# Kernel optimization log

Measured on AMD Instinct MI355X. Metric: run time of the kernel, lower is better.

Reference implementation:

```python
import jax, jax.numpy as jnp
import numpy as np

NEG_SLOPE = 0.01  # torch.nn.LeakyReLU default


def setup_inputs() -> dict:
    key = jax.random.key(0)
    ks = jax.random.split(key, 9)
    B, S, F1, F2, N, M, E, L = 2, 256, 512, 512, 20000, 2, 320000, 3
    x = jax.random.normal(ks[0], (B, S, F1), dtype=jnp.float32)
    nodes = jax.random.normal(ks[1], (N, M, F2), dtype=jnp.float32)
    edge_index = jax.random.randint(ks[2], (2, E), 0, N, dtype=jnp.int32)
    Wp = jax.random.normal(ks[3], (F1, F2), dtype=jnp.float32) * 0.02  # torch Linear weight [out,in]
    bp = jax.random.normal(ks[4], (F1,), dtype=jnp.float32) * 0.02
    gcn_W = jax.random.normal(ks[5], (L, S, S), dtype=jnp.float32) * 0.05  # stored as [in,out]
    gcn_b = jax.random.normal(ks[6], (L, S), dtype=jnp.float32) * 0.02
    w_bp = jax.random.normal(ks[7], (S,), dtype=jnp.float32) * 0.05
    b_bp = jax.random.normal(ks[8], (1,), dtype=jnp.float32) * 0.02
    return {"x": x, "nodes": nodes, "edge_index": edge_index, "Wp": Wp, "bp": bp,
            "gcn_W": gcn_W, "gcn_b": gcn_b, "w_bp": w_bp, "b_bp": b_bp}


def reference(x, nodes, edge_index, Wp, bp, gcn_W, gcn_b, w_bp, b_bp):
    # Eval mode: dropout layers are identity.
    N = nodes.shape[0]
    L = gcn_W.shape[0]
    proj = nodes @ Wp.T + bp                         # [N, M, F1]
    score = jnp.einsum('bsk,nmk->bsn', x, proj)      # sum over M and F1 -> [B, S, N]
    h = score.transpose(0, 2, 1)                     # beliefs [B, N, S]

    # GCN normalization with self-loops: D^{-1/2} (A + I) D^{-1/2}
    src, dst = edge_index[0], edge_index[1]
    loop = jnp.arange(N, dtype=edge_index.dtype)
    row = jnp.concatenate([src, loop])               # message sources
    col = jnp.concatenate([dst, loop])               # message targets
    deg = jnp.zeros((N,), dtype=h.dtype).at[col].add(1.0)
    dinv = deg ** -0.5                               # deg >= 1 due to self-loops
    norm = dinv[row] * dinv[col]                     # [E+N]

    for l in range(L):
        hw = h @ gcn_W[l]                            # [B, N, S]
        msg = hw[:, row, :] * norm[None, :, None]    # gather + scale
        agg = jnp.zeros_like(hw).at[:, col, :].add(msg) + gcn_b[l]
        h = jax.nn.leaky_relu(agg, NEG_SLOPE)

    # belief_projection: Linear(S, 1) then squeeze -> [B, N]
    return h @ w_bp + b_bp[0]
```

## Files before the change

### kernel.cpp

```cpp
#include <hip/hip_runtime.h>
#include <cstddef>
#include <cstdint>

#define NN 20000

typedef short frag16 __attribute__((ext_vector_type(8)));
typedef float f32x4 __attribute__((ext_vector_type(4)));

__device__ inline unsigned short f32_to_bf16(float f) {
    uint32_t u = __float_as_uint(f);
    u += 0x7FFFu + ((u >> 16) & 1u);
    return (unsigned short)(u >> 16);
}

__device__ inline void dec8_add(uint4 v, float* a) {
    a[0] += __uint_as_float(v.x << 16);
    a[1] += __uint_as_float(v.x & 0xffff0000u);
    a[2] += __uint_as_float(v.y << 16);
    a[3] += __uint_as_float(v.y & 0xffff0000u);
    a[4] += __uint_as_float(v.z << 16);
    a[5] += __uint_as_float(v.z & 0xffff0000u);
    a[6] += __uint_as_float(v.w << 16);
    a[7] += __uint_as_float(v.w & 0xffff0000u);
}

__global__ __launch_bounds__(256) void prep(
    const float* __restrict__ nodes, const float* __restrict__ x,
    const float* __restrict__ gcn_W, const float* __restrict__ bp,
    const int* __restrict__ src, const int* __restrict__ dst,
    unsigned short* __restrict__ nsum16, unsigned short* __restrict__ WT,
    float* __restrict__ Tf, float* __restrict__ cvec,
    int* __restrict__ cnt, int* __restrict__ csr, int E)
{
    __shared__ __align__(16) char shmem[8704];
    const int blk = blockIdx.x, tid = threadIdx.x;

    if (blk < 64) {
        float* As = (float*)shmem;
        float* Bs = As + 1024;
        int t = blk;
        int b = t >> 5, rem = t & 31;
        int s0 = (rem >> 3) * 64, f0 = (rem & 7) * 64;
        const float* W1 = gcn_W;
        const float* xb = x + (size_t)b * 256 * 512;
        int kk = tid >> 4, c4 = (tid & 15) << 2;
        int tm = tid >> 4, tn = tid & 15;
        float acc[4][4] = {};
        float4 av = *(const float4*)(W1 + (size_t)kk * 256 + s0 + c4);
        float4 bv = *(const float4*)(xb + (size_t)kk * 512 + f0 + c4);
        for (int k0 = 0; k0 < 256; k0 += 16) {
            __syncthreads();
            *(float4*)&As[kk * 64 + c4] = av;
            *(float4*)&Bs[kk * 64 + c4] = bv;
            __syncthreads();
            if (k0 + 16 < 256) {
                av = *(const float4*)(W1 + (size_t)(k0 + 16 + kk) * 256 + s0 + c4);
                bv = *(const float4*)(xb + (size_t)(k0 + 16 + kk) * 512 + f0 + c4);
            }
            #pragma unroll
            for (int k = 0; k < 16; ++k) {
                float a[4], bb[4];
                *(float4*)a  = *(const float4*)&As[k * 64 + (tm << 2)];
                *(float4*)bb = *(const float4*)&Bs[k * 64 + (tn << 2)];
                #pragma unroll
                for (int i = 0; i < 4; ++i)
                    #pragma unroll
                    for (int j = 0; j < 4; ++j) acc[i][j] += a[i] * bb[j];
            }
        }
        #pragma unroll
        for (int i = 0; i < 4; ++i) {
            int row = b * 256 + s0 + (tm << 2) + i;
            *(float4*)(Tf + (size_t)row * 512 + f0 + (tn << 2)) =
                make_float4(acc[i][0], acc[i][1], acc[i][2], acc[i][3]);
        }
    } else if (blk < 96) {
        unsigned short (*tsh)[68] = (unsigned short(*)[68])shmem;
        int t = blk - 64;
        int l = t >> 4, rem = t & 15;
        int c0 = (rem & 3) * 64, r0 = (rem >> 2) * 64;
        const float* inp = gcn_W + (size_t)(l + 1) * 65536;
        unsigned short* outp = WT + (size_t)l * 65536;
        int tx = tid & 15, ty = tid >> 4;
        #pragma unroll
        for (int rr = 0; rr < 4; ++rr) {
            int r = ty * 4 + rr;
            float4 v = *(const float4*)(inp + (size_t)(r0 + r) * 256 + c0 + tx * 4);
            tsh[tx * 4 + 0][r] = f32_to_bf16(v.x);
            tsh[tx * 4 + 1][r] = f32_to_bf16(v.y);
            tsh[tx * 4 + 2][r] = f32_to_bf16(v.z);
            tsh[tx * 4 + 3][r] = f32_to_bf16(v.w);
        }
        __syncthreads();
        #pragma unroll
        for (int cc = 0; cc < 4; ++cc) {
            int c = ty * 4 + cc;
            ushort4 o = *(ushort4*)&tsh[c][tx * 4];
            *(ushort4*)(outp + (size_t)(c0 + c) * 256 + r0 + tx * 4) = o;
        }
    } else if (blk < 224) {
        int row = (blk - 96) * 4 + (tid >> 6);
        int lane = tid & 63;
        const float* xr = x + (size_t)row * 512;
        float s = 0.f;
        #pragma unroll
        for (int k = 0; k < 512; k += 64) s += xr[k + lane] * bp[k + lane];
        #pragma unroll
        for (int off = 32; off; off >>= 1) s += __shfl_down(s, off);
        if (lane == 0) cvec[row] = 2.0f * s;
    } else if (blk < 224 + 2512) {
        int g = (blk - 224) * 256 + tid;
        int n = g >> 5, c = (g & 31) << 4;
        uint4 o0, o1;
        if (n < NN) {
            const float* r0 = nodes + (size_t)n * 1024 + c;
            const float* r1 = r0 + 512;
            float4 a0 = *(const float4*)(r0 + 0),  a1 = *(const float4*)(r0 + 4);
            float4 a2 = *(const float4*)(r0 + 8),  a3 = *(const float4*)(r0 + 12);
            float4 b0 = *(const float4*)(r1 + 0),  b1 = *(const float4*)(r1 + 4);
            float4 b2 = *(const float4*)(r1 + 8),  b3 = *(const float4*)(r1 + 12);
            o0.x = ((uint32_t)f32_to_bf16(a0.y + b0.y) << 16) | f32_to_bf16(a0.x + b0.x);
            o0.y = ((uint32_t)f32_to_bf16(a0.w + b0.w) << 16) | f32_to_bf16(a0.z + b0.z);
            o0.z = ((uint32_t)f32_to_bf16(a1.y + b1.y) << 16) | f32_to_bf16(a1.x + b1.x);
            o0.w = ((uint32_t)f32_to_bf16(a1.w + b1.w) << 16) | f32_to_bf16(a1.z + b1.z);
            o1.x = ((uint32_t)f32_to_bf16(a2.y + b2.y) << 16) | f32_to_bf16(a2.x + b2.x);
            o1.y = ((uint32_t)f32_to_bf16(a2.w + b2.w) << 16) | f32_to_bf16(a2.z + b2.z);
            o1.z = ((uint32_t)f32_to_bf16(a3.y + b3.y) << 16) | f32_to_bf16(a3.x + b3.x);
            o1.w = ((uint32_t)f32_to_bf16(a3.w + b3.w) << 16) | f32_to_bf16(a3.z + b3.z);
        } else {
            o0 = make_uint4(0, 0, 0, 0); o1 = o0;
        }
        *(uint4*)(nsum16 + (size_t)n * 512 + c) = o0;
        *(uint4*)(nsum16 + (size_t)n * 512 + c + 8) = o1;
    } else {
        int e = (blk - 2736) * 256 + tid;
        if (e < E) {
            int d = dst[e];
            int pos = atomicAdd(&cnt[d], 1);
            if (pos < 64) csr[(d << 6) + pos] = src[e];
        }
    }
}

__global__ __launch_bounds__(256) void mid(
    const float* __restrict__ Tf, const float* __restrict__ Wp,
    const float* __restrict__ gcn_W, const float* __restrict__ cvec,
    unsigned short* __restrict__ Ub, float* __restrict__ cb2)
{
    const int blk = blockIdx.x, tid = threadIdx.x;
    if (blk >= 256) {
        int idx = (blk - 256) * 256 + tid;
        int b = idx >> 8, s = idx & 255;
        float sum = 0.f;
        for (int sp = 0; sp < 256; ++sp)
            sum += gcn_W[(size_t)sp * 256 + s] * cvec[b * 256 + sp];
        cb2[idx] = sum;
        return;
    }
    __shared__ float As[16][33];
    __shared__ float Bs[16][34];
    int bm = (blk >> 4) << 5, bn = (blk & 15) << 5;
    int ar = tid >> 3, ac = (tid & 7) << 1;
    int br = tid >> 4, bc = (tid & 15) << 1;
    int tm = (tid >> 4) << 1, tn = (tid & 15) << 1;
    float acc[2][2] = {};
    for (int k0 = 0; k0 < 512; k0 += 16) {
        float2 av = *(const float2*)(Tf + (size_t)(bm + ar) * 512 + k0 + ac);
        float2 bv = *(const float2*)(Wp + (size_t)(k0 + br) * 512 + bn + bc);
        __syncthreads();
        As[ac][ar] = av.x; As[ac + 1][ar] = av.y;
        Bs[br][bc] = bv.x; Bs[br][bc + 1] = bv.y;
        __syncthreads();
        #pragma unroll
        for (int k = 0; k < 16; ++k) {
            float a0 = As[k][tm], a1 = As[k][tm + 1];
            float b0 = Bs[k][tn], b1 = Bs[k][tn + 1];
            acc[0][0] += a0 * b0; acc[0][1] += a0 * b1;
            acc[1][0] += a1 * b0; acc[1][1] += a1 * b1;
        }
    }
    #pragma unroll
    for (int i = 0; i < 2; ++i) {
        ushort2 o;
        o.x = f32_to_bf16(acc[i][0]); o.y = f32_to_bf16(acc[i][1]);
        *(ushort2*)(Ub + (size_t)(bm + tm + i) * 512 + bn + tn) = o;
    }
}

__global__ __launch_bounds__(256) void mgemm(
    const unsigned short* __restrict__ A, const unsigned short* __restrict__ BT,
    int K, int N, int mode,
    const float* __restrict__ cb2, const int* __restrict__ cnt,
    unsigned short* __restrict__ C)
{
    __shared__ __align__(16) unsigned short As[128 * 32];
    __shared__ __align__(16) unsigned short Bs[128 * 32];
    const int nwg = gridDim.x;
    const int orig = blockIdx.x;
    const int xcd = orig & 7, jj = orig >> 3;
    const int q = nwg >> 3, r = nwg & 7;
    const int wgid = (xcd < r ? xcd * (q + 1) : r * (q + 1) + (xcd - r) * q) + jj;
    const int lx = (mode == 1) ? 2 : 1;
    const int bm = (wgid >> lx) * 128, bn = (wgid & ((1 << lx) - 1)) * 128;
    const int tid = threadIdx.x;
    const int lane = tid & 63, w = tid >> 6;
    const int wm = (w >> 1) << 6, wn = (w & 1) << 6;
    const int r16 = lane & 15, q16 = lane >> 4;

    f32x4 acc[4][4] = {};

    for (int k0 = 0; k0 < K; k0 += 32) {
        __syncthreads();
        #pragma unroll
        for (int t = 0; t < 2; ++t) {
            int c = t * 256 + w * 64 + lane;
            int row = c >> 2, col = (c & 3) << 3;
            __builtin_amdgcn_global_load_lds(
                (const __attribute__((address_space(1))) void*)(A + (size_t)(bm + row) * K + k0 + col),
                (__attribute__((address_space(3))) void*)(As + (size_t)(t * 256 + w * 64) * 8),
                16, 0, 0);
            __builtin_amdgcn_global_load_lds(
                (const __attribute__((address_space(1))) void*)(BT + (size_t)(bn + row) * K + k0 + col),
                (__attribute__((address_space(3))) void*)(Bs + (size_t)(t * 256 + w * 64) * 8),
                16, 0, 0);
        }
        __syncthreads();
        frag16 af[4], bf[4];
        #pragma unroll
        for (int i = 0; i < 4; ++i)
            af[i] = *(const frag16*)(As + ((wm + i * 16 + r16) << 5) + (q16 << 3));
        #pragma unroll
        for (int j = 0; j < 4; ++j)
            bf[j] = *(const frag16*)(Bs + ((wn + j * 16 + r16) << 5) + (q16 << 3));
        #pragma unroll
        for (int i = 0; i < 4; ++i)
            #pragma unroll
            for (int j = 0; j < 4; ++j)
                acc[i][j] = __builtin_amdgcn_mfma_f32_16x16x32_bf16(af[i], bf[j], acc[i][j], 0, 0, 0);
    }

    #pragma unroll
    for (int i = 0; i < 4; ++i) {
        #pragma unroll
        for (int rg = 0; rg < 4; ++rg) {
            int m = bm + wm + i * 16 + (q16 << 2) + rg;
            float sc;
            int b2 = 0, node = m;
            if (mode == 1) {
                int nc = m > NN - 1 ? NN - 1 : m;
                sc = rsqrtf((float)cnt[nc] + 1.0f);
            } else {
                b2 = m >= NN;
                node = m - b2 * NN;
                int nc = node > NN - 1 ? NN - 1 : node;
                sc = rsqrtf((float)cnt[nc] + 1.0f);
                if (node > 20095) node = 20095;
            }
            #pragma unroll
            for (int j = 0; j < 4; ++j) {
                int n = bn + wn + j * 16 + r16;
                if (mode == 1) {
                    float v = (acc[i][j][rg] + cb2[n]) * sc;
                    C[(size_t)m * 512 + n] = f32_to_bf16(v);
                } else {
                    float v = acc[i][j][rg] * sc;
                    C[(size_t)node * 512 + (b2 << 8) + n] = f32_to_bf16(v);
                }
            }
        }
    }
}

__global__ __launch_bounds__(256) void aggregate_x(
    const unsigned short* __restrict__ hw, const int* __restrict__ cnt,
    const int* __restrict__ csr, const float* __restrict__ bias,
    unsigned short* __restrict__ hout,
    const float* __restrict__ w_bp, float* __restrict__ pout)
{
    __shared__ int sidx[2048];
    __shared__ int sdeg[32];
    const int s  = blockIdx.x & 7;
    const int nb = blockIdx.x >> 3;
    const int tid = threadIdx.x;
    const int g = tid >> 3;
    const int j = tid & 7;
    const int n = nb * 32 + g;

    {
        const int4* cp = (const int4*)(csr + ((size_t)nb << 11));
        int4 v0 = cp[tid * 2];
        int4 v1 = cp[tid * 2 + 1];
        *(int4*)&sidx[tid * 8]     = v0;
        *(int4*)&sidx[tid * 8 + 4] = v1;
        if (tid < 32) {
            int d = cnt[nb * 32 + tid];
            sdeg[tid] = d > 64 ? 64 : d;
        }
    }
    __syncthreads();

    const unsigned short* rowp = hw + (s << 6) + (j << 3);
    const int deg = sdeg[g];
    const int* gi = sidx + (g << 6);

    float acc[8] = {};
    dec8_add(*(const uint4*)(rowp + (size_t)n * 512), acc);

    int e = 0;
    for (; e + 8 <= deg; e += 8) {
        int s0 = gi[e + 0], s1 = gi[e + 1], s2 = gi[e + 2], s3 = gi[e + 3];
        int s4 = gi[e + 4], s5 = gi[e + 5], s6 = gi[e + 6], s7 = gi[e + 7];
        uint4 u0 = *(const uint4*)(rowp + (size_t)s0 * 512);
        uint4 u1 = *(const uint4*)(rowp + (size_t)s1 * 512);
        uint4 u2 = *(const uint4*)(rowp + (size_t)s2 * 512);
        uint4 u3 = *(const uint4*)(rowp + (size_t)s3 * 512);
        uint4 u4 = *(const uint4*)(rowp + (size_t)s4 * 512);
        uint4 u5 = *(const uint4*)(rowp + (size_t)s5 * 512);
        uint4 u6 = *(const uint4*)(rowp + (size_t)s6 * 512);
        uint4 u7 = *(const uint4*)(rowp + (size_t)s7 * 512);
        dec8_add(u0, acc); dec8_add(u1, acc); dec8_add(u2, acc); dec8_add(u3, acc);
        dec8_add(u4, acc); dec8_add(u5, acc); dec8_add(u6, acc); dec8_add(u7, acc);
    }
    for (; e < deg; ++e) {
        dec8_add(*(const uint4*)(rowp + (size_t)gi[e] * 512), acc);
    }

    float dn = rsqrtf((float)deg + 1.0f);
    int colb = ((s & 3) << 6) + (j << 3);
    float bl[8];
    *(float4*)&bl[0] = *(const float4*)(bias + colb);
    *(float4*)&bl[4] = *(const float4*)(bias + colb + 4);
    float v[8];
    #pragma unroll
    for (int t = 0; t < 8; ++t) {
        v[t] = fmaf(dn, acc[t], bl[t]);
        v[t] = v[t] > 0.f ? v[t] : 0.01f * v[t];
    }

    if (hout) {
        int b = s >> 2;
        uint4 o;
        o.x = ((uint32_t)f32_to_bf16(v[1]) << 16) | f32_to_bf16(v[0]);
        o.y = ((uint32_t)f32_to_bf16(v[3]) << 16) | f32_to_bf16(v[2]);
        o.z = ((uint32_t)f32_to_bf16(v[5]) << 16) | f32_to_bf16(v[4]);
        o.w = ((uint32_t)f32_to_bf16(v[7]) << 16) | f32_to_bf16(v[6]);
        *(uint4*)(hout + ((size_t)(b * NN + n)) * 256 + colb) = o;
    } else {
        float w4[8];
        *(float4*)&w4[0] = *(const float4*)(w_bp + colb);
        *(float4*)&w4[4] = *(const float4*)(w_bp + colb + 4);
        float sum = 0.f;
        #pragma unroll
        for (int t = 0; t < 8; ++t) sum += v[t] * w4[t];
        sum += __shfl_xor(sum, 1);
        sum += __shfl_xor(sum, 2);
        sum += __shfl_xor(sum, 4);
        if (j == 0) pout[s * NN + n] = sum;
    }
}

__global__ __launch_bounds__(256) void finishk(
    const float* __restrict__ pout, const float* __restrict__ b_bp,
    float* __restrict__ out)
{
    int i = blockIdx.x * 256 + threadIdx.x;
    if (i < 2 * NN) {
        int b = i >= NN;
        int n = i - b * NN;
        const float* p = pout + b * 4 * NN + n;
        out[i] = b_bp[0] + p[0] + p[NN] + p[2 * NN] + p[3 * NN];
    }
}

extern "C" void kernel_launch(void* const* d_in, const int* in_sizes, int n_in,
                              void* d_out, int out_size, void* d_ws, size_t ws_size,
                              hipStream_t stream) {
    const float* x     = (const float*)d_in[0];
    const float* nodes = (const float*)d_in[1];
    const int*   eidx  = (const int*)d_in[2];
    const float* Wp    = (const float*)d_in[3];
    const float* bp    = (const float*)d_in[4];
    const float* gcn_W = (const float*)d_in[5];
    const float* gcn_b = (const float*)d_in[6];
    const float* w_bp  = (const float*)d_in[7];
    const float* b_bp  = (const float*)d_in[8];
    const int E = in_sizes[2] / 2;

    char* w = (char*)d_ws;
    auto alloc = [&](size_t bytes) { char* p = w; w += (bytes + 255) & ~(size_t)255; return p; };
    unsigned short* nsum16 = (unsigned short*)alloc((size_t)20096 * 512 * 2);
    unsigned short* hw16   = (unsigned short*)alloc((size_t)20096 * 512 * 2);
    unsigned short* hA     = (unsigned short*)alloc((size_t)40192 * 256 * 2);
    unsigned short* hB     = (unsigned short*)alloc((size_t)40192 * 256 * 2);
    float* Tf  = (float*)alloc((size_t)512 * 512 * 4);
    unsigned short* Ub = (unsigned short*)alloc((size_t)512 * 512 * 2);
    unsigned short* WT = (unsigned short*)alloc((size_t)2 * 256 * 256 * 2);
    float* cvec = (float*)alloc(512 * 4);
    float* cb2  = (float*)alloc(512 * 4);
    float* pout = (float*)alloc((size_t)8 * NN * 4);
    int*   cnt  = (int*)alloc((size_t)NN * 4);
    int*   csr  = (int*)alloc((size_t)NN * 64 * 4);

    hipMemsetAsync(cnt, 0, (size_t)NN * 4, stream);

    const int cntBlks = (E + 255) / 256;
    prep<<<cntBlks + 64 + 2512 + 32 + 128, 256, 0, stream>>>(
        nodes, x, gcn_W, bp, eidx, eidx + E, nsum16, WT, Tf, cvec, cnt, csr, E);
    mid<<<258, 256, 0, stream>>>(Tf, Wp, gcn_W, cvec, Ub, cb2);

    mgemm<<<628, 256, 0, stream>>>(nsum16, Ub, 512, 512, 1, cb2, cnt, hw16);

    aggregate_x<<<5000, 256, 0, stream>>>(hw16, cnt, csr, gcn_b + 0, hA, w_bp, pout);
    mgemm<<<626, 256, 0, stream>>>(hA, WT, 256, 256, 2, nullptr, cnt, hw16);
    aggregate_x<<<5000, 256, 0, stream>>>(hw16, cnt, csr, gcn_b + 256, hB, w_bp, pout);
    mgemm<<<626, 256, 0, stream>>>(hB, WT + 65536, 256, 256, 2, nullptr, cnt, hw16);
    aggregate_x<<<5000, 256, 0, stream>>>(hw16, cnt, csr, gcn_b + 512, nullptr, w_bp, pout);
    finishk<<<157, 256, 0, stream>>>(pout, b_bp, (float*)d_out);
}
```

Baseline: 345.6 us.

## Shrink mgemm tile to 128x64, swizzle LDS layout, use 2D grid

Narrows the mgemm output tile from 128x128 to 128x64, which halves the B tile and the accumulator registers per thread and roughly doubles the number of workgroups. It adds an XOR swizzle on LDS chunk columns to avoid bank conflicts when fragments are read. It also replaces the XCD-aware block remapping with a plain 2D grid. The trade-off is less operand reuse per tile and the loss of the XCD locality mapping, in exchange for more parallelism and occupancy.

```diff
diff --git a/kernel.cpp b/kernel.cpp
--- a/kernel.cpp
+++ b/kernel.cpp
@@ -194,48 +194,52 @@
     unsigned short* __restrict__ C)
 {
     __shared__ __align__(16) unsigned short As[128 * 32];
-    __shared__ __align__(16) unsigned short Bs[128 * 32];
-    const int nwg = gridDim.x;
-    const int orig = blockIdx.x;
-    const int xcd = orig & 7, jj = orig >> 3;
-    const int q = nwg >> 3, r = nwg & 7;
-    const int wgid = (xcd < r ? xcd * (q + 1) : r * (q + 1) + (xcd - r) * q) + jj;
-    const int lx = (mode == 1) ? 2 : 1;
-    const int bm = (wgid >> lx) * 128, bn = (wgid & ((1 << lx) - 1)) * 128;
+    __shared__ __align__(16) unsigned short Bs[64 * 32];
+    const int bm = blockIdx.y * 128, bn = blockIdx.x * 64;
     const int tid = threadIdx.x;
     const int lane = tid & 63, w = tid >> 6;
-    const int wm = (w >> 1) << 6, wn = (w & 1) << 6;
+    const int wm = (w >> 1) << 6, wn = (w & 1) << 5;
     const int r16 = lane & 15, q16 = lane >> 4;
 
-    f32x4 acc[4][4] = {};
+    f32x4 acc[4][2] = {};
 
     for (int k0 = 0; k0 < K; k0 += 32) {
         __syncthreads();
-        #pragma unroll
-        for (int t = 0; t < 2; ++t) {
-            int c = t * 256 + w * 64 + lane;
-            int row = c >> 2, col = (c & 3) << 3;
+        {
+            #pragma unroll
+            for (int t = 0; t < 2; ++t) {
+                int c = t * 256 + w * 64 + lane;
+                int row = c >> 2, cb = c & 3;
+                int gcol = (cb ^ (row & 3)) << 3;
+                __builtin_amdgcn_global_load_lds(
+                    (const __attribute__((address_space(1))) void*)(A + (size_t)(bm + row) * K + k0 + gcol),
+                    (__attribute__((address_space(3))) void*)(As + (size_t)(t * 256 + w * 64) * 8),
+                    16, 0, 0);
+            }
+            int c = w * 64 + lane;
+            int row = c >> 2, cb = c & 3;
+            int gcol = (cb ^ (row & 3)) << 3;
             __builtin_amdgcn_global_load_lds(
-                (const __attribute__((address_space(1))) void*)(A + (size_t)(bm + row) * K + k0 + col),
-                (__attribute__((address_space(3))) void*)(As + (size_t)(t * 256 + w * 64) * 8),
+                (const __attribute__((address_space(1))) void*)(BT + (size_t)(bn + row) * K + k0 + gcol),
+                (__attribute__((address_space(3))) void*)(Bs + (size_t)(w * 64) * 8),
                 16, 0, 0);
-            __builtin_amdgcn_global_load_lds(
-                (const __attribute__((address_space(1))) void*)(BT + (size_t)(bn + row) * K + k0 + col),
-                (__attribute__((address_space(3))) void*)(Bs + (size_t)(t * 256 + w * 64) * 8),
-                16, 0, 0);
         }
         __syncthreads();
-        frag16 af[4], bf[4];
-        #pragma unroll
-        for (int i = 0; i < 4; ++i)
-            af[i] = *(const frag16*)(As + ((wm + i * 16 + r16) << 5) + (q16 << 3));
-        #pragma unroll
-        for (int j = 0; j < 4; ++j)
-            bf[j] = *(const frag16*)(Bs + ((wn + j * 16 + r16) << 5) + (q16 << 3));
+        frag16 af[4], bf[2];
+        #pragma unroll
+        for (int i = 0; i < 4; ++i) {
+            int ra = wm + i * 16 + r16;
+            af[i] = *(const frag16*)(As + (ra << 5) + ((q16 ^ (ra & 3)) << 3));
+        }
+        #pragma unroll
+        for (int j = 0; j < 2; ++j) {
+            int rb = wn + j * 16 + r16;
+            bf[j] = *(const frag16*)(Bs + (rb << 5) + ((q16 ^ (rb & 3)) << 3));
+        }
         #pragma unroll
         for (int i = 0; i < 4; ++i)
             #pragma unroll
-            for (int j = 0; j < 4; ++j)
+            for (int j = 0; j < 2; ++j)
                 acc[i][j] = __builtin_amdgcn_mfma_f32_16x16x32_bf16(af[i], bf[j], acc[i][j], 0, 0, 0);
     }
 
@@ -257,7 +261,7 @@
                 if (node > 20095) node = 20095;
             }
             #pragma unroll
-            for (int j = 0; j < 4; ++j) {
+            for (int j = 0; j < 2; ++j) {
                 int n = bn + wn + j * 16 + r16;
                 if (mode == 1) {
                     float v = (acc[i][j][rg] + cb2[n]) * sc;
@@ -408,12 +412,12 @@
         nodes, x, gcn_W, bp, eidx, eidx + E, nsum16, WT, Tf, cvec, cnt, csr, E);
     mid<<<258, 256, 0, stream>>>(Tf, Wp, gcn_W, cvec, Ub, cb2);
 
-    mgemm<<<628, 256, 0, stream>>>(nsum16, Ub, 512, 512, 1, cb2, cnt, hw16);
+    mgemm<<<dim3(8, 157), 256, 0, stream>>>(nsum16, Ub, 512, 512, 1, cb2, cnt, hw16);
 
     aggregate_x<<<5000, 256, 0, stream>>>(hw16, cnt, csr, gcn_b + 0, hA, w_bp, pout);
-    mgemm<<<626, 256, 0, stream>>>(hA, WT, 256, 256, 2, nullptr, cnt, hw16);
+    mgemm<<<dim3(4, 314), 256, 0, stream>>>(hA, WT, 256, 256, 2, nullptr, cnt, hw16);
     aggregate_x<<<5000, 256, 0, stream>>>(hw16, cnt, csr, gcn_b + 256, hB, w_bp, pout);
-    mgemm<<<626, 256, 0, stream>>>(hB, WT + 65536, 256, 256, 2, nullptr, cnt, hw16);
+    mgemm<<<dim3(4, 314), 256, 0, stream>>>(hB, WT + 65536, 256, 256, 2, nullptr, cnt, hw16);
     aggregate_x<<<5000, 256, 0, stream>>>(hw16, cnt, csr, gcn_b + 512, nullptr, w_bp, pout);
     finishk<<<157, 256, 0, stream>>>(pout, b_bp, (float*)d_out);
 }
```

Result: no change. 352.0 us (+1.8%).
